# Performance work log

Hardware: AMD Instinct MI355X
Metric: run time of the kernel (lower is better)

## Reference

```python
import jax, jax.numpy as jnp
import numpy as np

B, M, N, DIM, P, Q, OUT = 64, 64, 64, 3, 3, 3, 512


def gen_knot_vector(p, n):
    # p leading zeros + linspace(0,1,n-p) + p trailing ones (repo convention)
    return np.concatenate([np.zeros(p), np.linspace(0.0, 1.0, n - p), np.ones(p)])


def precompute_basis(n_ctrl, p, out_dim):
    """Knot spans and Cox-de Boor basis values (Piegl A2.1/A2.2) on a uniform param grid."""
    U = gen_knot_vector(p, n_ctrl)
    u = np.linspace(0.0, 1.0, out_dim)
    # largest i with U[i] <= u, clamped to the valid span range [p, n_ctrl-2]
    spans = np.clip(np.searchsorted(U, u, side='right') - 1, p, n_ctrl - 2)
    Nmat = np.zeros((out_dim, p + 1))
    for i in range(out_dim):
        s, uu = int(spans[i]), u[i]
        Ni = np.zeros(p + 1); Ni[0] = 1.0
        left = np.zeros(p + 1); right = np.zeros(p + 1)
        for j in range(1, p + 1):
            left[j] = uu - U[s + 1 - j]
            right[j] = U[s + j] - uu
            saved = 0.0
            for r in range(j):
                temp = Ni[r] / (right[r + 1] + left[j - r])
                Ni[r] = saved + right[r + 1] * temp
                saved = left[j - r] * temp
            Ni[j] = saved
        Nmat[i] = Ni
    # gather index table: control-point row span-p+l for l in 0..p
    idx = spans[:, None] - p + np.arange(p + 1)[None, :]
    return Nmat.astype(np.float32), idx.astype(np.int64)


def setup_inputs() -> dict:
    key = jax.random.key(0)
    k1, k2 = jax.random.split(key)
    xyz = jax.random.normal(k1, (B, M, N, DIM), dtype=jnp.float32)
    w = jax.random.uniform(k2, (B, M, N, 1), dtype=jnp.float32, minval=0.5, maxval=1.5)
    ctrl = jnp.concatenate([xyz, w], axis=-1)  # homogeneous control points [B,M,N,4]
    Nu, iu = precompute_basis(M, P, OUT)
    Nv, iv = precompute_basis(N, Q, OUT)
    return {"ctrl": ctrl, "Nu": jnp.asarray(Nu), "Nv": jnp.asarray(Nv),
            "iu": jnp.asarray(iu), "iv": jnp.asarray(iv)}


def reference(ctrl, Nu, Nv, iu, iv):
    D = ctrl.shape[-1] - 1
    U_, V_ = Nu.shape[0], Nv.shape[0]
    surf = jnp.zeros((ctrl.shape[0], U_, V_, ctrl.shape[-1]), dtype=ctrl.dtype)
    for l in range(iu.shape[1]):          # p+1 terms (fixed, small)
        rows = ctrl[:, iu[:, l]]          # [B, U, N, D+1]
        for r in range(iv.shape[1]):      # q+1 terms (fixed, small)
            pts = rows[:, :, iv[:, r]]    # [B, U, V, D+1]
            w = Nu[:, l][:, None] * Nv[None, :, r]  # [U, V]
            surf = surf + w[None, :, :, None] * pts
    return surf[..., :D] / surf[..., D:]  # perspective divide
```

## Files before the change

kernel.cpp:

```cpp
#include <hip/hip_runtime.h>


#define OUTDIM 512
#define CTRL_N 64
#define TU 8

__global__ __launch_bounds__(256) void surf_eval_kernel(
    const float* __restrict__ ctrl,
    const float* __restrict__ Nu,
    const float* __restrict__ Nv,
    const int*   __restrict__ iu,
    const int*   __restrict__ iv,
    float*       __restrict__ out)
{
    __shared__ float4 rows[TU * CTRL_N];

    const int blk = blockIdx.x;
    const int b  = blk >> 6;
    const int U0 = (blk & 63) * TU;
    const int t  = threadIdx.x;

    {
        const int u  = t >> 5;
        const int n0 = t & 31;
        const int U  = U0 + u;
        const float4 nu  = *(const float4*)(Nu + U * 4);
        const int4   iu4 = *(const int4*)(iu + U * 4);
        const float* cb = ctrl + (size_t)b * (64 * 64 * 4);
        const float* r0 = cb + (size_t)iu4.x * (CTRL_N * 4);
        const float* r1 = cb + (size_t)iu4.y * (CTRL_N * 4);
        const float* r2 = cb + (size_t)iu4.z * (CTRL_N * 4);
        const float* r3 = cb + (size_t)iu4.w * (CTRL_N * 4);

#pragma unroll
        for (int k = 0; k < 2; ++k) {
            const int n = n0 + 32 * k;
            const float4 p0 = *(const float4*)(r0 + n * 4);
            const float4 p1 = *(const float4*)(r1 + n * 4);
            const float4 p2 = *(const float4*)(r2 + n * 4);
            const float4 p3 = *(const float4*)(r3 + n * 4);
            float4 acc;
            acc.x = nu.x * p0.x + nu.y * p1.x + nu.z * p2.x + nu.w * p3.x;
            acc.y = nu.x * p0.y + nu.y * p1.y + nu.z * p2.y + nu.w * p3.y;
            acc.z = nu.x * p0.z + nu.y * p1.z + nu.z * p2.z + nu.w * p3.z;
            acc.w = nu.x * p0.w + nu.y * p1.w + nu.z * p2.w + nu.w * p3.w;
            rows[u * CTRL_N + n] = acc;
        }
    }
    __syncthreads();

    const int v0 = t << 1;
    const float4 nvA = *(const float4*)(Nv + v0 * 4);
    const int4   ivA = *(const int4*)(iv + v0 * 4);
    const float4 nvB = *(const float4*)(Nv + v0 * 4 + 4);
    const int4   ivB = *(const int4*)(iv + v0 * 4 + 4);

    float* ob = out + (((size_t)b * OUTDIM + U0) * OUTDIM + v0) * 3;

#pragma unroll
    for (int u = 0; u < TU; ++u) {
        const float4* ru = rows + u * CTRL_N;

        const float4 a0 = ru[ivA.x];
        const float4 a1 = ru[ivA.y];
        const float4 a2 = ru[ivA.z];
        const float4 a3 = ru[ivA.w];
        const float4 b0 = ru[ivB.x];
        const float4 b1 = ru[ivB.y];
        const float4 b2 = ru[ivB.z];
        const float4 b3 = ru[ivB.w];

        float sxA = nvA.x * a0.x + nvA.y * a1.x + nvA.z * a2.x + nvA.w * a3.x;
        float syA = nvA.x * a0.y + nvA.y * a1.y + nvA.z * a2.y + nvA.w * a3.y;
        float szA = nvA.x * a0.z + nvA.y * a1.z + nvA.z * a2.z + nvA.w * a3.z;
        float swA = nvA.x * a0.w + nvA.y * a1.w + nvA.z * a2.w + nvA.w * a3.w;

        float sxB = nvB.x * b0.x + nvB.y * b1.x + nvB.z * b2.x + nvB.w * b3.x;
        float syB = nvB.x * b0.y + nvB.y * b1.y + nvB.z * b2.y + nvB.w * b3.y;
        float szB = nvB.x * b0.z + nvB.y * b1.z + nvB.z * b2.z + nvB.w * b3.z;
        float swB = nvB.x * b0.w + nvB.y * b1.w + nvB.z * b2.w + nvB.w * b3.w;

        const float invA = __builtin_amdgcn_rcpf(swA);
        const float invB = __builtin_amdgcn_rcpf(swB);

        float* po = ob + u * (OUTDIM * 3);
        *(float2*)(po + 0) = make_float2(sxA * invA, syA * invA);
        *(float2*)(po + 2) = make_float2(szA * invA, sxB * invB);
        *(float2*)(po + 4) = make_float2(syB * invB, szB * invB);
    }
}

extern "C" void kernel_launch(void* const* d_in, const int* in_sizes, int n_in,
                              void* d_out, int out_size, void* d_ws, size_t ws_size,
                              hipStream_t stream) {
    const float* ctrl = (const float*)d_in[0];
    const float* Nu   = (const float*)d_in[1];
    const float* Nv   = (const float*)d_in[2];
    const int*   iu   = (const int*)d_in[3];
    const int*   iv   = (const int*)d_in[4];
    float* out = (float*)d_out;

    const int nblocks = 64 * (OUTDIM / TU);
    surf_eval_kernel<<<nblocks, 256, 0, stream>>>(ctrl, Nu, Nv, iu, iv, out);
}
```

Baseline: 209.6 us.

## Stage output rows in LDS for coalesced float4 stores and share span loads

Each thread now exploits the fact that adjacent outputs v0 and v0+1 have spans that differ by at most one. It loads five consecutive control rows instead of eight gathered ones and applies shifted weights for the second point. Results are staged in a double-buffered LDS array so each output row is written with contiguous float4 stores instead of strided float2 stores. This adds a barrier per row and extra LDS traffic, and it relies on the span-step assumption holding for this knot layout.

```diff
diff --git a/kernel.cpp b/kernel.cpp
--- a/kernel.cpp
+++ b/kernel.cpp
@@ -14,6 +14,7 @@
     float*       __restrict__ out)
 {
     __shared__ float4 rows[TU * CTRL_N];
+    __shared__ __align__(16) float stg[2][OUTDIM * 3];
 
     const int blk = blockIdx.x;
     const int b  = blk >> 6;
@@ -51,42 +52,57 @@
 
     const int v0 = t << 1;
     const float4 nvA = *(const float4*)(Nv + v0 * 4);
-    const int4   ivA = *(const int4*)(iv + v0 * 4);
     const float4 nvB = *(const float4*)(Nv + v0 * 4 + 4);
-    const int4   ivB = *(const int4*)(iv + v0 * 4 + 4);
+    const int    iA  = iv[v0 * 4];
+    const int    dB  = iv[v0 * 4 + 4] - iA;
 
-    float* ob = out + (((size_t)b * OUTDIM + U0) * OUTDIM + v0) * 3;
+    const float wB0 = dB ? 0.0f  : nvB.x;
+    const float wB1 = dB ? nvB.x : nvB.y;
+    const float wB2 = dB ? nvB.y : nvB.z;
+    const float wB3 = dB ? nvB.z : nvB.w;
+    const float wB4 = dB ? nvB.w : 0.0f;
 
-#pragma unroll
-    for (int u = 0; u < TU; ++u) {
+    float* orow = out + ((size_t)b * OUTDIM + U0) * (OUTDIM * 3);
+
+    auto compute_and_stage = [&](int u) {
         const float4* ru = rows + u * CTRL_N;
+        const float4 q0 = ru[iA + 0];
+        const float4 q1 = ru[iA + 1];
+        const float4 q2 = ru[iA + 2];
+        const float4 q3 = ru[iA + 3];
+        const float4 q4 = ru[iA + 4];
 
-        const float4 a0 = ru[ivA.x];
-        const float4 a1 = ru[ivA.y];
-        const float4 a2 = ru[ivA.z];
-        const float4 a3 = ru[ivA.w];
-        const float4 b0 = ru[ivB.x];
-        const float4 b1 = ru[ivB.y];
-        const float4 b2 = ru[ivB.z];
-        const float4 b3 = ru[ivB.w];
+        float sxA = nvA.x * q0.x + nvA.y * q1.x + nvA.z * q2.x + nvA.w * q3.x;
+        float syA = nvA.x * q0.y + nvA.y * q1.y + nvA.z * q2.y + nvA.w * q3.y;
+        float szA = nvA.x * q0.z + nvA.y * q1.z + nvA.z * q2.z + nvA.w * q3.z;
+        float swA = nvA.x * q0.w + nvA.y * q1.w + nvA.z * q2.w + nvA.w * q3.w;
 
-        float sxA = nvA.x * a0.x + nvA.y * a1.x + nvA.z * a2.x + nvA.w * a3.x;
-        float syA = nvA.x * a0.y + nvA.y * a1.y + nvA.z * a2.y + nvA.w * a3.y;
-        float szA = nvA.x * a0.z + nvA.y * a1.z + nvA.z * a2.z + nvA.w * a3.z;
-        float swA = nvA.x * a0.w + nvA.y * a1.w + nvA.z * a2.w + nvA.w * a3.w;
-
-        float sxB = nvB.x * b0.x + nvB.y * b1.x + nvB.z * b2.x + nvB.w * b3.x;
-        float syB = nvB.x * b0.y + nvB.y * b1.y + nvB.z * b2.y + nvB.w * b3.y;
-        float szB = nvB.x * b0.z + nvB.y * b1.z + nvB.z * b2.z + nvB.w * b3.z;
-        float swB = nvB.x * b0.w + nvB.y * b1.w + nvB.z * b2.w + nvB.w * b3.w;
+        float sxB = wB0 * q0.x + wB1 * q1.x + wB2 * q2.x + wB3 * q3.x + wB4 * q4.x;
+        float syB = wB0 * q0.y + wB1 * q1.y + wB2 * q2.y + wB3 * q3.y + wB4 * q4.y;
+        float szB = wB0 * q0.z + wB1 * q1.z + wB2 * q2.z + wB3 * q3.z + wB4 * q4.z;
+        float swB = wB0 * q0.w + wB1 * q1.w + wB2 * q2.w + wB3 * q3.w + wB4 * q4.w;
 
         const float invA = __builtin_amdgcn_rcpf(swA);
         const float invB = __builtin_amdgcn_rcpf(swB);
 
-        float* po = ob + u * (OUTDIM * 3);
-        *(float2*)(po + 0) = make_float2(sxA * invA, syA * invA);
-        *(float2*)(po + 2) = make_float2(szA * invA, sxB * invB);
-        *(float2*)(po + 4) = make_float2(syB * invB, szB * invB);
+        float2* sp = (float2*)&stg[u & 1][6 * t];
+        sp[0] = make_float2(sxA * invA, syA * invA);
+        sp[1] = make_float2(szA * invA, sxB * invB);
+        sp[2] = make_float2(syB * invB, szB * invB);
+    };
+
+    compute_and_stage(0);
+
+#pragma unroll
+    for (int u = 0; u < TU; ++u) {
+        __syncthreads();
+        if (u + 1 < TU) compute_and_stage(u + 1);
+
+        const float4* sb = (const float4*)stg[u & 1];
+        float* og = orow + u * (OUTDIM * 3);
+        *(float4*)(og + 4 * t) = sb[t];
+        if (t < 128)
+            *(float4*)(og + 4 * (256 + t)) = sb[256 + t];
     }
 }
 
```

Measured after the change: 206.0 us. About the same (-1.7%).
